# Performance work log

Measured on AMD Instinct MI355X. Metric: run time of the kernel, lower is better.

The kernel has to match this reference:

```python
import jax, jax.numpy as jnp
import numpy as np

H = 8          # num_heads
DK = 64        # head dim (head_size // num_heads)
SPARSITY = 0.5 # pre-softmax random drop probability
DROPOUT = 0.1  # post-softmax dropout probability


def setup_inputs() -> dict:
    key = jax.random.key(0)
    ks = jax.random.split(key, 12)
    B, S, D = 4, 2048, 512
    mk = lambda k, shp, scale=1.0: (jax.random.normal(k, shp, dtype=jnp.float32) * scale)
    return {
        "query": mk(ks[0], (B, S, D)),
        "key": mk(ks[1], (B, S, D)),
        "value": mk(ks[2], (B, S, D)),
        "Wq": mk(ks[3], (D, D), 0.04),
        "bq": mk(ks[4], (D,), 0.02),
        "Wk": mk(ks[5], (D, D), 0.04),
        "bk": mk(ks[6], (D,), 0.02),
        "Wv": mk(ks[7], (D, D), 0.04),
        "bv": mk(ks[8], (D,), 0.02),
        "Wo": mk(ks[9], (D, D), 0.04),
        "bo": mk(ks[10], (D,), 0.02),
    }


def _split_heads(x, B):
    # [B, S, H*DK] -> [B, H, S, DK]
    return x.reshape(B, -1, H, DK).transpose(0, 2, 1, 3)


def reference(query, key, value, Wq, bq, Wk, bk, Wv, bv, Wo, bo):
    B, S, D = query.shape
    # q/k/v projections (torch Linear: x @ W.T + b)
    q = _split_heads(query @ Wq.T + bq, B)   # [B, H, S, DK]
    k = _split_heads(key @ Wk.T + bk, B)
    v = _split_heads(value @ Wv.T + bv, B)

    scores = jnp.einsum("bhqd,bhkd->bhqk", q, k) / jnp.sqrt(jnp.float32(DK))

    # random pre-softmax sparsity mask: keep where U(0,1) > sparsity
    mkey = jax.random.fold_in(jax.random.key(42), 1)
    keep_sparse = jax.random.uniform(mkey, scores.shape) > SPARSITY
    scores = jnp.where(keep_sparse, scores, -jnp.inf)

    p_attn = jax.nn.softmax(scores, axis=-1)

    # dropout on attention probs, inverted scaling as in torch
    dkey = jax.random.fold_in(jax.random.key(42), 2)
    keep_drop = jax.random.uniform(dkey, p_attn.shape) >= DROPOUT
    p_attn = jnp.where(keep_drop, p_attn / (1.0 - DROPOUT), 0.0)

    x = jnp.einsum("bhqk,bhkd->bhqd", p_attn, v)        # [B, H, S, DK]
    x = x.transpose(0, 2, 1, 3).reshape(B, S, H * DK)    # [B, S, D]
    return x @ Wo.T + bo
```

## Files before the change

kernel.cpp:

```cpp
#include <hip/hip_runtime.h>
#include <stdint.h>

#define BATCH  4
#define SQ     2048
#define DMODEL 512
#define NH     8
#define DK     64

typedef __attribute__((ext_vector_type(8))) short short8;
typedef __attribute__((ext_vector_type(4))) float f32x4;

struct TFK { uint32_t a, b; };
constexpr uint32_t rotl_ce(uint32_t x, int d) {
  return (x << d) | (x >> (32 - d));
}
constexpr TFK tf_ce(uint32_t k0, uint32_t k1, uint32_t x0, uint32_t x1) {
  const uint32_t ks[3] = {k0, k1, k0 ^ k1 ^ 0x1BD11BDAu};
  const int rot[2][4] = {{13, 15, 26, 6}, {17, 29, 16, 24}};
  x0 += k0; x1 += k1;
  for (int c = 0; c < 5; ++c) {
    for (int j = 0; j < 4; ++j) {
      x0 += x1; x1 = rotl_ce(x1, rot[c & 1][j]); x1 ^= x0;
    }
    x0 += ks[(c + 1) % 3];
    x1 += ks[(c + 2) % 3] + (uint32_t)(c + 1);
  }
  return TFK{x0, x1};
}
constexpr TFK SPK = tf_ce(0u, 42u, 0u, 1u);
constexpr TFK DPK = tf_ce(0u, 42u, 0u, 2u);

template <uint32_t K0, uint32_t K1>
__device__ __forceinline__ uint32_t tf_bits(uint32_t ctr) {
  constexpr uint32_t KS2 = K0 ^ K1 ^ 0x1BD11BDAu;
  uint32_t x0 = K0;
  uint32_t x1 = K1 + ctr;
#define RND(d) { x0 += x1; x1 = __builtin_amdgcn_alignbit(x1, x1, 32 - (d)); x1 ^= x0; }
  RND(13) RND(15) RND(26) RND(6)
  x0 += K1; x1 += KS2 + 1u;
  RND(17) RND(29) RND(16) RND(24)
  x0 += KS2; x1 += K0 + 2u;
  RND(13) RND(15) RND(26) RND(6)
  x0 += K0; x1 += K1 + 3u;
  RND(17) RND(29) RND(16) RND(24)
  x0 += K1; x1 += KS2 + 4u;
  RND(13) RND(15) RND(26) RND(6)
  x0 += KS2; x1 += K0 + 5u;
#undef RND
  return x0 ^ x1;
}

#define SP_THR 0x80000200u
#define DP_THR 0x1999A200u

__device__ __forceinline__ ushort f2bf_rne(float f) {
  uint32_t u = __float_as_uint(f);
  return (ushort)((u + 0x7fffu + ((u >> 16) & 1u)) >> 16);
}
__device__ __forceinline__ float bf2f(ushort h) {
  return __uint_as_float((uint32_t)h << 16);
}

__device__ __forceinline__ void split4(const float *__restrict__ src,
                                       ushort *__restrict__ dh,
                                       ushort *__restrict__ dl, size_t base) {
  float4 x = *(const float4 *)(src + base);
  uint32_t h[4], lo[4];
#pragma unroll
  for (int i = 0; i < 4; ++i) {
    float xi = ((const float *)&x)[i];
    ushort hh = f2bf_rne(xi);
    h[i] = hh;
    lo[i] = f2bf_rne(xi - bf2f(hh));
  }
  uint2 ph, pl;
  ph.x = h[0] | (h[1] << 16);  ph.y = h[2] | (h[3] << 16);
  pl.x = lo[0] | (lo[1] << 16); pl.y = lo[2] | (lo[3] << 16);
  *(uint2 *)(dh + base) = ph;
  *(uint2 *)(dl + base) = pl;
}

__global__ __launch_bounds__(256) void split_inputs_k(
    const float *__restrict__ q, const float *__restrict__ k,
    const float *__restrict__ v, ushort *__restrict__ qh,
    ushort *__restrict__ ql, ushort *__restrict__ kh, ushort *__restrict__ kl,
    ushort *__restrict__ vh, ushort *__restrict__ vl) {
  const float *src = blockIdx.y == 0 ? q : (blockIdx.y == 1 ? k : v);
  ushort *dh = blockIdx.y == 0 ? qh : (blockIdx.y == 1 ? kh : vh);
  ushort *dl = blockIdx.y == 0 ? ql : (blockIdx.y == 1 ? kl : vl);
  const size_t base = ((size_t)blockIdx.x * 256 + threadIdx.x) * 4;
  split4(src, dh, dl, base);
}

__global__ __launch_bounds__(256) void split_w_k(
    const float *__restrict__ w0, const float *__restrict__ w1,
    const float *__restrict__ w2, const float *__restrict__ w3,
    ushort *__restrict__ h0, ushort *__restrict__ l0, ushort *__restrict__ h1,
    ushort *__restrict__ l1, ushort *__restrict__ h2, ushort *__restrict__ l2,
    ushort *__restrict__ h3, ushort *__restrict__ l3) {
  const int y = blockIdx.y;
  const float *src = y == 0 ? w0 : (y == 1 ? w1 : (y == 2 ? w2 : w3));
  ushort *dh = y == 0 ? h0 : (y == 1 ? h1 : (y == 2 ? h2 : h3));
  ushort *dl = y == 0 ? l0 : (y == 1 ? l1 : (y == 2 ? l2 : l3));
  const size_t base = ((size_t)blockIdx.x * 256 + threadIdx.x) * 4;
  split4(src, dh, dl, base);
}

template <int MODE>
__global__ __launch_bounds__(256) void proj_mfma(
    const ushort *__restrict__ Ah, const ushort *__restrict__ Al,
    const ushort *__restrict__ Bh, const ushort *__restrict__ Bl,
    const float *__restrict__ bias, void *__restrict__ Yv) {
  const int tid = threadIdx.x;
  const int w = tid >> 6, l = tid & 63;
  const int lr = l & 15, lq = l >> 4;
  const int am = blockIdx.y * 128 + w * 32;
  const int bn = blockIdx.x * 64;
  f32x4 acc[2][4];
#pragma unroll
  for (int i = 0; i < 2; ++i)
#pragma unroll
    for (int j = 0; j < 4; ++j) acc[i][j] = (f32x4){0.f, 0.f, 0.f, 0.f};

#pragma unroll 2
  for (int k0 = 0; k0 < DMODEL; k0 += 32) {
    short8 ah[2], al[2], bh[4], bl[4];
#pragma unroll
    for (int mf = 0; mf < 2; ++mf) {
      const size_t off = (size_t)(am + mf * 16 + lr) * DMODEL + k0 + lq * 8;
      ah[mf] = *(const short8 *)(Ah + off);
      al[mf] = *(const short8 *)(Al + off);
    }
#pragma unroll
    for (int nf = 0; nf < 4; ++nf) {
      const size_t off = (size_t)(bn + nf * 16 + lr) * DMODEL + k0 + lq * 8;
      bh[nf] = *(const short8 *)(Bh + off);
      bl[nf] = *(const short8 *)(Bl + off);
    }
#pragma unroll
    for (int mf = 0; mf < 2; ++mf)
#pragma unroll
      for (int nf = 0; nf < 4; ++nf) {
        acc[mf][nf] = __builtin_amdgcn_mfma_f32_16x16x32_bf16(
            ah[mf], bh[nf], acc[mf][nf], 0, 0, 0);
        acc[mf][nf] = __builtin_amdgcn_mfma_f32_16x16x32_bf16(
            ah[mf], bl[nf], acc[mf][nf], 0, 0, 0);
        acc[mf][nf] = __builtin_amdgcn_mfma_f32_16x16x32_bf16(
            al[mf], bh[nf], acc[mf][nf], 0, 0, 0);
      }
  }

#pragma unroll
  for (int mf = 0; mf < 2; ++mf)
#pragma unroll
    for (int nf = 0; nf < 4; ++nf) {
      if (MODE == 0) {
        float *Y = (float *)Yv;
        const int gn = bn + nf * 16 + lr;
        const float bb = bias[gn];
#pragma unroll
        for (int r = 0; r < 4; ++r) {
          const int gm = am + mf * 16 + lq * 4 + r;
          Y[(size_t)gm * DMODEL + gn] = acc[mf][nf][r] + bb;
        }
      } else if (MODE == 1) {
        ushort *Y = (ushort *)Yv;
        const int gn = bn + nf * 16 + lr;
        const float bb = bias[gn];
#pragma unroll
        for (int r = 0; r < 4; ++r) {
          const int gm = am + mf * 16 + lq * 4 + r;
          Y[(size_t)gm * DMODEL + gn] = f2bf_rne(acc[mf][nf][r] + bb);
        }
      } else {
        ushort *Y = (ushort *)Yv;
        const int gm2 = bn + nf * 16 + lr;
        const int bcol = gm2 >> 11, scol = gm2 & 2047;
#pragma unroll
        for (int r = 0; r < 4; ++r) {
          const int gn2 = am + mf * 16 + lq * 4 + r;
          Y[((size_t)(bcol * DMODEL + gn2)) * SQ + scol] =
              f2bf_rne(acc[mf][nf][r] + bias[gn2]);
        }
      }
    }
}

__global__ __launch_bounds__(256, 2) void attn_mfma(
    const ushort *__restrict__ qp, const ushort *__restrict__ kp,
    const ushort *__restrict__ vpt, ushort *__restrict__ xah,
    ushort *__restrict__ xal) {
  __shared__ __align__(16) uint8_t lds[24576];
  uint8_t *Ks = lds;
  uint8_t *Vt = lds + 8192;
  const int b = blockIdx.z, h = blockIdx.y;
  const int qb = blockIdx.x * 64;
  const int tid = threadIdx.x;
  const int w = tid >> 6, l = tid & 63;
  const int lr = l & 15, lq = l >> 4;
  uint8_t *Ps = lds + 16384 + w * 2048;
  const int bh = b * NH + h;

  short8 qf[2];
  {
    const int qrow = qb + w * 16 + lr;
    const ushort *qrowp = qp + ((size_t)(b * SQ + qrow)) * DMODEL + h * DK;
    qf[0] = *(const short8 *)(qrowp + lq * 8);
    qf[1] = *(const short8 *)(qrowp + 32 + lq * 8);
  }
  f32x4 o[4];
  f32x4 lacc;
#pragma unroll
  for (int nd = 0; nd < 4; ++nd) o[nd] = (f32x4){0.f, 0.f, 0.f, 0.f};
  lacc = (f32x4){0.f, 0.f, 0.f, 0.f};

  uint32_t rowflat[4];
#pragma unroll
  for (int r = 0; r < 4; ++r)
    rowflat[r] = ((uint32_t)(bh * SQ + qb + w * 16 + lq * 4 + r)) << 11;

  for (int kv = 0; kv < SQ; kv += 64) {
    __syncthreads();
    {
      const int row = tid >> 2;
      const int c0 = (tid & 3) * 2;
      const int sw = (row & 7) << 4;
      const ushort *ksrc =
          kp + ((size_t)(b * SQ + kv + row)) * DMODEL + h * DK + c0 * 8;
      uint4 d0 = *(const uint4 *)ksrc;
      uint4 d1 = *(const uint4 *)(ksrc + 8);
      *(uint4 *)(Ks + ((row * 128 + c0 * 16) ^ sw)) = d0;
      *(uint4 *)(Ks + ((row * 128 + (c0 + 1) * 16) ^ sw)) = d1;
      const ushort *vsrc = vpt + ((size_t)(bh * DK + row)) * SQ + kv + c0 * 8;
      uint4 e0 = *(const uint4 *)vsrc;
      uint4 e1 = *(const uint4 *)(vsrc + 8);
      *(uint4 *)(Vt + ((row * 128 + c0 * 16) ^ sw)) = e0;
      *(uint4 *)(Vt + ((row * 128 + (c0 + 1) * 16) ^ sw)) = e1;
    }
    __syncthreads();

    f32x4 s[4];
#pragma unroll
    for (int ni = 0; ni < 4; ++ni) s[ni] = (f32x4){0.f, 0.f, 0.f, 0.f};
#pragma unroll
    for (int ni = 0; ni < 4; ++ni) {
      const int krow = ni * 16 + lr;
      const int sw = (krow & 7) << 4;
#pragma unroll
      for (int kf = 0; kf < 2; ++kf) {
        short8 kb =
            *(const short8 *)(Ks + ((krow * 128 + kf * 64 + lq * 16) ^ sw));
        s[ni] = __builtin_amdgcn_mfma_f32_16x16x32_bf16(qf[kf], kb, s[ni], 0, 0, 0);
      }
    }

#pragma unroll
    for (int ni = 0; ni < 4; ++ni) {
#pragma unroll
      for (int r = 0; r < 4; ++r) {
        const uint32_t ctr = rowflat[r] + (uint32_t)(kv + ni * 16 + lr);
        const bool keep_s = tf_bits<SPK.a, SPK.b>(ctr) >= SP_THR;
        const bool keep_d = tf_bits<DPK.a, DPK.b>(ctr) >= DP_THR;
        float e = __expf(s[ni][r] * 0.125f);
        float p = keep_s ? e : 0.0f;
        lacc[r] += p;
        float pd = keep_d ? p * (1.0f / 0.9f) : 0.0f;
        const int prow = lq * 4 + r;
        *(ushort *)(Ps + ((prow * 128 + (ni * 16 + lr) * 2) ^ ((prow & 7) << 4))) =
            f2bf_rne(pd);
      }
    }

#pragma unroll
    for (int kf = 0; kf < 2; ++kf) {
      short8 pa = *(const short8 *)(Ps +
                                    ((lr * 128 + kf * 64 + lq * 16) ^ ((lr & 7) << 4)));
#pragma unroll
      for (int nd = 0; nd < 4; ++nd) {
        const int vrow = nd * 16 + lr;
        short8 vb = *(const short8 *)(Vt + ((vrow * 128 + kf * 64 + lq * 16) ^
                                            ((vrow & 7) << 4)));
        o[nd] = __builtin_amdgcn_mfma_f32_16x16x32_bf16(pa, vb, o[nd], 0, 0, 0);
      }
    }
  }

  float inv[4];
#pragma unroll
  for (int r = 0; r < 4; ++r) {
    float t = lacc[r];
    t += __shfl_xor(t, 1);
    t += __shfl_xor(t, 2);
    t += __shfl_xor(t, 4);
    t += __shfl_xor(t, 8);
    inv[r] = 1.0f / t;
  }
#pragma unroll
  for (int nd = 0; nd < 4; ++nd)
#pragma unroll
    for (int r = 0; r < 4; ++r) {
      const int qrow = qb + w * 16 + lq * 4 + r;
      const size_t idx =
          ((size_t)(b * SQ + qrow)) * DMODEL + h * DK + nd * 16 + lr;
      const float val = o[nd][r] * inv[r];
      const ushort hh = f2bf_rne(val);
      xah[idx] = hh;
      xal[idx] = f2bf_rne(val - bf2f(hh));
    }
}

extern "C" void kernel_launch(void *const *d_in, const int *in_sizes, int n_in,
                              void *d_out, int out_size, void *d_ws,
                              size_t ws_size, hipStream_t stream) {
  (void)in_sizes; (void)n_in; (void)out_size;
  const float *query = (const float *)d_in[0];
  const float *key_  = (const float *)d_in[1];
  const float *value = (const float *)d_in[2];
  const float *Wq = (const float *)d_in[3];
  const float *bq = (const float *)d_in[4];
  const float *Wk = (const float *)d_in[5];
  const float *bk = (const float *)d_in[6];
  const float *Wv = (const float *)d_in[7];
  const float *bv = (const float *)d_in[8];
  const float *Wo = (const float *)d_in[9];
  const float *bo = (const float *)d_in[10];
  float *out = (float *)d_out;

  const size_t MB = (size_t)1 << 20;
  if (ws_size < 92 * MB) return;

  char *ws = (char *)d_ws;
  ushort *qih = (ushort *)(ws);
  ushort *qil = (ushort *)(ws + 8 * MB);
  ushort *kih = (ushort *)(ws + 16 * MB);
  ushort *kil = (ushort *)(ws + 24 * MB);
  ushort *vih = (ushort *)(ws + 32 * MB);
  ushort *vil = (ushort *)(ws + 40 * MB);
  ushort *Wqh = (ushort *)(ws + 48 * MB);
  ushort *Wql = (ushort *)(ws + 48 * MB + 512 * 1024);
  ushort *Wkh = (ushort *)(ws + 49 * MB);
  ushort *Wkl = (ushort *)(ws + 49 * MB + 512 * 1024);
  ushort *Wvh = (ushort *)(ws + 50 * MB);
  ushort *Wvl = (ushort *)(ws + 50 * MB + 512 * 1024);
  ushort *Woh = (ushort *)(ws + 51 * MB);
  ushort *Wol = (ushort *)(ws + 51 * MB + 512 * 1024);
  ushort *qp  = (ushort *)(ws + 52 * MB);
  ushort *kp  = (ushort *)(ws + 60 * MB);
  ushort *vpt = (ushort *)(ws + 68 * MB);
  ushort *xah = (ushort *)(ws + 76 * MB);
  ushort *xal = (ushort *)(ws + 84 * MB);

  split_inputs_k<<<dim3(4096, 3), 256, 0, stream>>>(query, key_, value, qih,
                                                    qil, kih, kil, vih, vil);
  split_w_k<<<dim3(256, 4), 256, 0, stream>>>(Wq, Wk, Wv, Wo, Wqh, Wql, Wkh,
                                              Wkl, Wvh, Wvl, Woh, Wol);

  proj_mfma<1><<<dim3(8, 64), 256, 0, stream>>>(qih, qil, Wqh, Wql, bq, qp);
  proj_mfma<1><<<dim3(8, 64), 256, 0, stream>>>(kih, kil, Wkh, Wkl, bk, kp);
  proj_mfma<2><<<dim3(128, 4), 256, 0, stream>>>(Wvh, Wvl, vih, vil, bv, vpt);

  attn_mfma<<<dim3(SQ / 64, NH, BATCH), 256, 0, stream>>>(qp, kp, vpt, xah,
                                                          xal);

  proj_mfma<0><<<dim3(8, 64), 256, 0, stream>>>(xah, xal, Woh, Wol, bo, out);
}
```

Before: 721.6 us.

## Double-buffer K/V tiles, runtime threefry keys, exp2 softmax, LDS-staged V transpose

The attention kernel now double-buffers K and V tiles in LDS. It issues global loads for the next tile before computing on the current one and keeps a single barrier per iteration. Threefry key constants become kernel arguments with pre-folded key injections, and exp is computed via the native exp2 builtin with a folded scale. The transposed V projection output is staged through shared memory so stores are coalesced 16-byte writes. The cost is more LDS use in attention (40KB), which may reduce occupancy, and an extra barrier in the projection.

```diff
diff --git a/kernel.cpp b/kernel.cpp
--- a/kernel.cpp
+++ b/kernel.cpp
@@ -30,28 +30,46 @@
 constexpr TFK SPK = tf_ce(0u, 42u, 0u, 1u);
 constexpr TFK DPK = tf_ce(0u, 42u, 0u, 2u);
 
-template <uint32_t K0, uint32_t K1>
-__device__ __forceinline__ uint32_t tf_bits(uint32_t ctr) {
-  constexpr uint32_t KS2 = K0 ^ K1 ^ 0x1BD11BDAu;
-  uint32_t x0 = K0;
-  uint32_t x1 = K1 + ctr;
-#define RND(d) { x0 += x1; x1 = __builtin_amdgcn_alignbit(x1, x1, 32 - (d)); x1 ^= x0; }
-  RND(13) RND(15) RND(26) RND(6)
-  x0 += K1; x1 += KS2 + 1u;
-  RND(17) RND(29) RND(16) RND(24)
-  x0 += KS2; x1 += K0 + 2u;
-  RND(13) RND(15) RND(26) RND(6)
-  x0 += K0; x1 += K1 + 3u;
-  RND(17) RND(29) RND(16) RND(24)
-  x0 += K1; x1 += KS2 + 4u;
-  RND(13) RND(15) RND(26) RND(6)
-  x0 += KS2; x1 += K0 + 5u;
-#undef RND
-  return x0 ^ x1;
-}
-
 #define SP_THR 0x80000200u
 #define DP_THR 0x1999A200u
+
+struct TfArgs {
+  uint32_t sp[8];
+  uint32_t dp[8];
+  uint32_t sp_thr, dp_thr;
+};
+
+__device__ __forceinline__ void tf_round(uint32_t &x0, uint32_t &x1, int d) {
+  x0 += x1;
+  x1 = __builtin_amdgcn_alignbit(x1, x1, 32 - d);
+  x1 ^= x0;
+}
+__device__ __forceinline__ void tf_grp(uint32_t &x0, uint32_t &x1,
+                                       uint32_t injx1, uint32_t injx0, int d0,
+                                       int d1, int d2, int d3) {
+  x1 += injx1;
+  x0 = x0 + injx0 + x1;
+  x1 = __builtin_amdgcn_alignbit(x1, x1, 32 - d0);
+  x1 ^= x0;
+  tf_round(x0, x1, d1);
+  tf_round(x0, x1, d2);
+  tf_round(x0, x1, d3);
+}
+__device__ __forceinline__ uint32_t tf_rt(const uint32_t *__restrict__ c,
+                                          uint32_t ctr) {
+  uint32_t x1 = c[1] + ctr;
+  uint32_t x0 = c[0] + x1;
+  x1 = __builtin_amdgcn_alignbit(x1, x1, 19);
+  x1 ^= x0;
+  tf_round(x0, x1, 15);
+  tf_round(x0, x1, 26);
+  tf_round(x0, x1, 6);
+  tf_grp(x0, x1, c[2], c[1], 17, 29, 16, 24);
+  tf_grp(x0, x1, c[3], c[7], 13, 15, 26, 6);
+  tf_grp(x0, x1, c[4], c[0], 17, 29, 16, 24);
+  tf_grp(x0, x1, c[5], c[1], 13, 15, 26, 6);
+  return (x0 + c[7]) ^ (x1 + c[6]);
+}
 
 __device__ __forceinline__ ushort f2bf_rne(float f) {
   uint32_t u = __float_as_uint(f);
@@ -59,6 +77,13 @@
 }
 __device__ __forceinline__ float bf2f(ushort h) {
   return __uint_as_float((uint32_t)h << 16);
+}
+__device__ __forceinline__ float exp_scaled(float s) {
+#if __has_builtin(__builtin_amdgcn_exp2f)
+  return __builtin_amdgcn_exp2f(s * 0.18033688011112042f);
+#else
+  return __expf(s * 0.125f);
+#endif
 }
 
 __device__ __forceinline__ void split4(const float *__restrict__ src,
@@ -111,6 +136,7 @@
     const ushort *__restrict__ Ah, const ushort *__restrict__ Al,
     const ushort *__restrict__ Bh, const ushort *__restrict__ Bl,
     const float *__restrict__ bias, void *__restrict__ Yv) {
+  __shared__ ushort Tt[MODE == 2 ? 128 * 72 : 1];
   const int tid = threadIdx.x;
   const int w = tid >> 6, l = tid & 63;
   const int lr = l & 15, lq = l >> 4;
@@ -150,38 +176,52 @@
       }
   }
 
+  if (MODE == 2) {
+#pragma unroll
+    for (int mf = 0; mf < 2; ++mf)
+#pragma unroll
+      for (int nf = 0; nf < 4; ++nf) {
+        const int gn2 = am + mf * 16 + lq * 4;
+#pragma unroll
+        for (int r = 0; r < 4; ++r) {
+          const int featl = (w * 32 + mf * 16 + lq * 4 + r);
+          Tt[featl * 72 + nf * 16 + lr] =
+              f2bf_rne(acc[mf][nf][r] + bias[gn2 + r]);
+        }
+      }
+    __syncthreads();
+    ushort *Y = (ushort *)Yv;
+    const int feat = tid >> 1, half = tid & 1;
+    const int gfeat = blockIdx.y * 128 + feat;
+    const int bcol = bn >> 11, scol = (bn & 2047) + half * 32;
+    ushort *dst = Y + ((size_t)(bcol * DMODEL + gfeat)) * SQ + scol;
+    const ushort *srcp = &Tt[feat * 72 + half * 32];
+#pragma unroll
+    for (int j = 0; j < 4; ++j)
+      *(uint4 *)(dst + j * 8) = *(const uint4 *)(srcp + j * 8);
+    return;
+  }
+
 #pragma unroll
   for (int mf = 0; mf < 2; ++mf)
 #pragma unroll
     for (int nf = 0; nf < 4; ++nf) {
+      const int gn = bn + nf * 16 + lr;
+      const float bb = bias[gn];
       if (MODE == 0) {
         float *Y = (float *)Yv;
-        const int gn = bn + nf * 16 + lr;
-        const float bb = bias[gn];
 #pragma unroll
         for (int r = 0; r < 4; ++r) {
           const int gm = am + mf * 16 + lq * 4 + r;
           Y[(size_t)gm * DMODEL + gn] = acc[mf][nf][r] + bb;
         }
-      } else if (MODE == 1) {
+      } else {
         ushort *Y = (ushort *)Yv;
-        const int gn = bn + nf * 16 + lr;
-        const float bb = bias[gn];
 #pragma unroll
         for (int r = 0; r < 4; ++r) {
           const int gm = am + mf * 16 + lq * 4 + r;
           Y[(size_t)gm * DMODEL + gn] = f2bf_rne(acc[mf][nf][r] + bb);
         }
-      } else {
-        ushort *Y = (ushort *)Yv;
-        const int gm2 = bn + nf * 16 + lr;
-        const int bcol = gm2 >> 11, scol = gm2 & 2047;
-#pragma unroll
-        for (int r = 0; r < 4; ++r) {
-          const int gn2 = am + mf * 16 + lq * 4 + r;
-          Y[((size_t)(bcol * DMODEL + gn2)) * SQ + scol] =
-              f2bf_rne(acc[mf][nf][r] + bias[gn2]);
-        }
       }
     }
 }
@@ -189,16 +229,14 @@
 __global__ __launch_bounds__(256, 2) void attn_mfma(
     const ushort *__restrict__ qp, const ushort *__restrict__ kp,
     const ushort *__restrict__ vpt, ushort *__restrict__ xah,
-    ushort *__restrict__ xal) {
-  __shared__ __align__(16) uint8_t lds[24576];
-  uint8_t *Ks = lds;
-  uint8_t *Vt = lds + 8192;
+    ushort *__restrict__ xal, TfArgs ta) {
+  __shared__ __align__(16) uint8_t lds[40960];
   const int b = blockIdx.z, h = blockIdx.y;
   const int qb = blockIdx.x * 64;
   const int tid = threadIdx.x;
   const int w = tid >> 6, l = tid & 63;
   const int lr = l & 15, lq = l >> 4;
-  uint8_t *Ps = lds + 16384 + w * 2048;
+  uint8_t *Ps = lds + 32768 + w * 2048;
   const int bh = b * NH + h;
 
   short8 qf[2];
@@ -219,25 +257,45 @@
   for (int r = 0; r < 4; ++r)
     rowflat[r] = ((uint32_t)(bh * SQ + qb + w * 16 + lq * 4 + r)) << 11;
 
+  const int srow = tid >> 2;
+  const int sc0 = (tid & 3) * 2;
+  const int ssw = (srow & 7) << 4;
+  const ushort *kbase =
+      kp + ((size_t)(b * SQ) + srow) * DMODEL + h * DK + sc0 * 8;
+  const ushort *vbase = vpt + ((size_t)(bh * DK + srow)) * SQ + sc0 * 8;
+  const int la0 = (srow * 128 + sc0 * 16) ^ ssw;
+  const int la1 = (srow * 128 + (sc0 + 1) * 16) ^ ssw;
+
+  uint4 kr0, kr1, vr0, vr1;
+#define ISSUE(kv_)                                            \
+  {                                                           \
+    const ushort *ks_ = kbase + (size_t)(kv_)*DMODEL;         \
+    kr0 = *(const uint4 *)ks_;                                \
+    kr1 = *(const uint4 *)(ks_ + 8);                          \
+    const ushort *vs_ = vbase + (kv_);                        \
+    vr0 = *(const uint4 *)vs_;                                \
+    vr1 = *(const uint4 *)(vs_ + 8);                          \
+  }
+#define STORE(buf_)                                           \
+  {                                                           \
+    uint8_t *Kb_ = lds + (buf_)*8192;                         \
+    uint8_t *Vb_ = lds + 16384 + (buf_)*8192;                 \
+    *(uint4 *)(Kb_ + la0) = kr0;                              \
+    *(uint4 *)(Kb_ + la1) = kr1;                              \
+    *(uint4 *)(Vb_ + la0) = vr0;                              \
+    *(uint4 *)(Vb_ + la1) = vr1;                              \
+  }
+
+  ISSUE(0)
+  STORE(0)
+  __syncthreads();
+
   for (int kv = 0; kv < SQ; kv += 64) {
-    __syncthreads();
-    {
-      const int row = tid >> 2;
-      const int c0 = (tid & 3) * 2;
-      const int sw = (row & 7) << 4;
-      const ushort *ksrc =
-          kp + ((size_t)(b * SQ + kv + row)) * DMODEL + h * DK + c0 * 8;
-      uint4 d0 = *(const uint4 *)ksrc;
-      uint4 d1 = *(const uint4 *)(ksrc + 8);
-      *(uint4 *)(Ks + ((row * 128 + c0 * 16) ^ sw)) = d0;
-      *(uint4 *)(Ks + ((row * 128 + (c0 + 1) * 16) ^ sw)) = d1;
-      const ushort *vsrc = vpt + ((size_t)(bh * DK + row)) * SQ + kv + c0 * 8;
-      uint4 e0 = *(const uint4 *)vsrc;
-      uint4 e1 = *(const uint4 *)(vsrc + 8);
-      *(uint4 *)(Vt + ((row * 128 + c0 * 16) ^ sw)) = e0;
-      *(uint4 *)(Vt + ((row * 128 + (c0 + 1) * 16) ^ sw)) = e1;
-    }
-    __syncthreads();
+    const int cur = (kv >> 6) & 1;
+    uint8_t *Ks = lds + cur * 8192;
+    uint8_t *Vt = lds + 16384 + cur * 8192;
+    const bool more = (kv + 64) < SQ;
+    if (more) ISSUE(kv + 64)
 
     f32x4 s[4];
 #pragma unroll
@@ -250,31 +308,34 @@
       for (int kf = 0; kf < 2; ++kf) {
         short8 kb =
             *(const short8 *)(Ks + ((krow * 128 + kf * 64 + lq * 16) ^ sw));
-        s[ni] = __builtin_amdgcn_mfma_f32_16x16x32_bf16(qf[kf], kb, s[ni], 0, 0, 0);
-      }
-    }
-
+        s[ni] =
+            __builtin_amdgcn_mfma_f32_16x16x32_bf16(qf[kf], kb, s[ni], 0, 0, 0);
+      }
+    }
+
+    const uint32_t colbase = (uint32_t)(kv + lr);
 #pragma unroll
     for (int ni = 0; ni < 4; ++ni) {
 #pragma unroll
       for (int r = 0; r < 4; ++r) {
-        const uint32_t ctr = rowflat[r] + (uint32_t)(kv + ni * 16 + lr);
-        const bool keep_s = tf_bits<SPK.a, SPK.b>(ctr) >= SP_THR;
-        const bool keep_d = tf_bits<DPK.a, DPK.b>(ctr) >= DP_THR;
-        float e = __expf(s[ni][r] * 0.125f);
+        const uint32_t ctr = rowflat[r] + colbase + (uint32_t)(ni * 16);
+        const bool keep_s = tf_rt(ta.sp, ctr) >= ta.sp_thr;
+        const bool keep_d = tf_rt(ta.dp, ctr) >= ta.dp_thr;
+        float e = exp_scaled(s[ni][r]);
         float p = keep_s ? e : 0.0f;
         lacc[r] += p;
         float pd = keep_d ? p * (1.0f / 0.9f) : 0.0f;
         const int prow = lq * 4 + r;
-        *(ushort *)(Ps + ((prow * 128 + (ni * 16 + lr) * 2) ^ ((prow & 7) << 4))) =
+        *(ushort *)(Ps +
+                    ((prow * 128 + (ni * 16 + lr) * 2) ^ ((prow & 7) << 4))) =
             f2bf_rne(pd);
       }
     }
 
 #pragma unroll
     for (int kf = 0; kf < 2; ++kf) {
-      short8 pa = *(const short8 *)(Ps +
-                                    ((lr * 128 + kf * 64 + lq * 16) ^ ((lr & 7) << 4)));
+      short8 pa = *(const short8 *)(Ps + ((lr * 128 + kf * 64 + lq * 16) ^
+                                          ((lr & 7) << 4)));
 #pragma unroll
       for (int nd = 0; nd < 4; ++nd) {
         const int vrow = nd * 16 + lr;
@@ -283,7 +344,12 @@
         o[nd] = __builtin_amdgcn_mfma_f32_16x16x32_bf16(pa, vb, o[nd], 0, 0, 0);
       }
     }
-  }
+
+    if (more) STORE(cur ^ 1)
+    __syncthreads();
+  }
+#undef ISSUE
+#undef STORE
 
   float inv[4];
 #pragma unroll
@@ -350,6 +416,15 @@
   ushort *xah = (ushort *)(ws + 76 * MB);
   ushort *xal = (ushort *)(ws + 84 * MB);
 
+  constexpr uint32_t KS2s = SPK.a ^ SPK.b ^ 0x1BD11BDAu;
+  constexpr uint32_t KS2d = DPK.a ^ DPK.b ^ 0x1BD11BDAu;
+  TfArgs ta = {
+      {SPK.a, SPK.b, KS2s + 1u, SPK.a + 2u, SPK.b + 3u, KS2s + 4u, SPK.a + 5u,
+       KS2s},
+      {DPK.a, DPK.b, KS2d + 1u, DPK.a + 2u, DPK.b + 3u, KS2d + 4u, DPK.a + 5u,
+       KS2d},
+      SP_THR, DP_THR};
+
   split_inputs_k<<<dim3(4096, 3), 256, 0, stream>>>(query, key_, value, qih,
                                                     qil, kih, kil, vih, vil);
   split_w_k<<<dim3(256, 4), 256, 0, stream>>>(Wq, Wk, Wv, Wo, Wqh, Wql, Wkh,
@@ -360,7 +435,7 @@
   proj_mfma<2><<<dim3(128, 4), 256, 0, stream>>>(Wvh, Wvl, vih, vil, bv, vpt);
 
   attn_mfma<<<dim3(SQ / 64, NH, BATCH), 256, 0, stream>>>(qp, kp, vpt, xah,
-                                                          xal);
+                                                          xal, ta);
 
   proj_mfma<0><<<dim3(8, 64), 256, 0, stream>>>(xah, xal, Woh, Wol, bo, out);
 }
```

Result: no change. 715.5 us (-0.9%).
